# Kernel optimization log

Hardware: AMD Instinct MI355X
Metric: run time of the kernel (lower is better)

## Reference

```python
import jax, jax.numpy as jnp
import numpy as np

NUM_ITERATIONS = 100
EPS = 1e-6
LIPSCHITZ_COEFF = 0.9


def _l2_normalize(x, axis=None, eps=1e-12):
    return x * jax.lax.rsqrt((x * x).sum(axis=axis, keepdims=True) + eps)


def setup_inputs() -> dict:
    key = jax.random.key(0)
    k1, k2, k3, k4 = jax.random.split(key, 4)
    B, D_in, D_out = 32768, 1024, 1024
    x = jax.random.normal(k1, (B, D_in), dtype=jnp.float32)
    # TruncatedNormal(stddev=1/sqrt(fan_in)) approximated by scaled normal
    w = jax.random.normal(k2, (D_in, D_out), dtype=jnp.float32) / np.sqrt(D_in)
    b = jax.random.normal(k3, (D_out,), dtype=jnp.float32)
    u0 = jax.random.normal(k4, (1, D_out), dtype=jnp.float32)
    return {"x": x, "w": w, "b": b, "u0": u0}


def reference(x, w, b, u0):
    d_in = w.shape[0]

    # 100-step power iteration: tight sequential dependency chain of GEMV pairs.
    def body(i, carry):
        u, _ = carry
        v = _l2_normalize(jnp.matmul(u, w.T), eps=EPS)   # [1, d_in]
        u = _l2_normalize(jnp.matmul(v, w), eps=EPS)     # [1, d_out]
        return (u, v)

    v_init = jnp.zeros((1, d_in), dtype=w.dtype)
    u, v = jax.lax.fori_loop(0, NUM_ITERATIONS, body, (u0, v_init))
    u = jax.lax.stop_gradient(u)
    v = jax.lax.stop_gradient(v)

    sigma = jnp.matmul(jnp.matmul(v, w), u.T)[0, 0]      # spectral norm estimate
    factor = jnp.maximum(1.0, sigma / LIPSCHITZ_COEFF)
    w_norm = w / factor

    out = jnp.dot(x, w_norm) + b
    return out
```

## Files before the change

kernel.cpp:

```cpp
#include <hip/hip_runtime.h>
#include <hip/hip_bf16.h>
#include <cstdint>
#include <cstddef>

#define DDIM 1024
#define BROWS 32768

typedef __attribute__((ext_vector_type(8))) short short8;
typedef __attribute__((ext_vector_type(4))) float floatx4;

__device__ __forceinline__ float bf2f(unsigned short u) {
  return __uint_as_float(((unsigned int)u) << 16);
}
__device__ __forceinline__ unsigned short f2bf(float f) {
  unsigned int u = __float_as_uint(f);
  u += 0x7FFFu + ((u >> 16) & 1u);
  return (unsigned short)(u >> 16);
}

__device__ __forceinline__ void load_lds16(const void* g, void* l) {
  __builtin_amdgcn_global_load_lds(
      (const __attribute__((address_space(1))) unsigned int*)g,
      (__attribute__((address_space(3))) unsigned int*)l,
      16, 0, 0);
}

__global__ void __launch_bounds__(512, 2)
big_gemm(const float* __restrict__ Af, const unsigned short* __restrict__ Bt,
         float* __restrict__ Outf, const float* __restrict__ inv_ptr,
         const float* __restrict__ bias)
{
  __shared__ __align__(16) char smem[49152];

  const int tid  = threadIdx.x;
  const int lane = tid & 63;
  const int wid  = tid >> 6;
  const int wr = wid >> 2, wc = wid & 3;
  const int g = lane >> 4, r = lane & 15;

  const int bm0 = (int)(blockIdx.x & 255) * 128;
  const int bn0 = (int)(blockIdx.x >> 8) * 256;

  const floatx4 zero4 = {0.f, 0.f, 0.f, 0.f};
  floatx4 acc[4][4];
#pragma unroll
  for (int m = 0; m < 4; ++m)
#pragma unroll
    for (int n = 0; n < 4; ++n) acc[m][n] = zero4;

  const int ao   = tid * 16;
  const int arow = ao >> 6;
  const int acol = (ao & 63) >> 1;
  const float* aSrc = Af + (size_t)(bm0 + arow) * DDIM + acol;

  {
#pragma unroll
    for (int p = 0; p < 2; ++p) {
      const int o = p * 8192 + tid * 16;
      const int row = o >> 6;
      const int cole = (o & 63) >> 1;
      load_lds16(Bt + (size_t)(bn0 + row) * DDIM + cole, smem + 16384 + o);
    }
    float4 x0 = *(const float4*)aSrc;
    float4 x1 = *(const float4*)(aSrc + 4);
    short8 t;
    t[0] = (short)f2bf(x0.x); t[1] = (short)f2bf(x0.y);
    t[2] = (short)f2bf(x0.z); t[3] = (short)f2bf(x0.w);
    t[4] = (short)f2bf(x1.x); t[5] = (short)f2bf(x1.y);
    t[6] = (short)f2bf(x1.z); t[7] = (short)f2bf(x1.w);
    *(short8*)(smem + ao) = t;
  }
  __syncthreads();

  for (int t = 0; t < 32; ++t) {
    const int co = t & 1;
    char* curA = smem + co * 8192;
    char* curB = smem + 16384 + co * 16384;
    char* nxtA = smem + (co ^ 1) * 8192;
    char* nxtB = smem + 16384 + (co ^ 1) * 16384;

    float4 pa0, pa1;
    const bool pref = (t < 31);
    if (pref) {
      const int ko = (t + 1) * 32;
#pragma unroll
      for (int p = 0; p < 2; ++p) {
        const int o = p * 8192 + tid * 16;
        const int row = o >> 6;
        const int cole = (o & 63) >> 1;
        load_lds16(Bt + (size_t)(bn0 + row) * DDIM + ko + cole, nxtB + o);
      }
      pa0 = *(const float4*)(aSrc + ko);
      pa1 = *(const float4*)(aSrc + ko + 4);
    }

    short8 afr[4], bfr[4];
#pragma unroll
    for (int m = 0; m < 4; ++m)
      afr[m] = *(const short8*)(curA + (wr * 64 + m * 16 + r) * 64 + g * 16);
#pragma unroll
    for (int n = 0; n < 4; ++n)
      bfr[n] = *(const short8*)(curB + (wc * 64 + n * 16 + r) * 64 + g * 16);
#pragma unroll
    for (int m = 0; m < 4; ++m)
#pragma unroll
      for (int n = 0; n < 4; ++n)
        acc[m][n] = __builtin_amdgcn_mfma_f32_16x16x32_bf16(afr[m], bfr[n], acc[m][n], 0, 0, 0);

    if (pref) {
      short8 tt;
      tt[0] = (short)f2bf(pa0.x); tt[1] = (short)f2bf(pa0.y);
      tt[2] = (short)f2bf(pa0.z); tt[3] = (short)f2bf(pa0.w);
      tt[4] = (short)f2bf(pa1.x); tt[5] = (short)f2bf(pa1.y);
      tt[6] = (short)f2bf(pa1.z); tt[7] = (short)f2bf(pa1.w);
      *(short8*)(nxtA + ao) = tt;
    }
    __syncthreads();
  }

  const float inv = *inv_ptr;
#pragma unroll
  for (int n = 0; n < 4; ++n) {
    const int ocol = bn0 + wc * 64 + n * 16 + r;
    const float bv = bias[ocol];
#pragma unroll
    for (int m = 0; m < 4; ++m) {
      const int orow0 = bm0 + wr * 64 + m * 16 + g * 4;
#pragma unroll
      for (int q = 0; q < 4; ++q) {
        Outf[(size_t)(orow0 + q) * DDIM + ocol] = acc[m][n][q] * inv + bv;
      }
    }
  }
}

__global__ void __launch_bounds__(256, 2)
sq_gemm(const unsigned short* __restrict__ A, const unsigned short* __restrict__ Bt,
        unsigned short* __restrict__ Out, const float* __restrict__ in_max,
        float* __restrict__ out_max)
{
  __shared__ __align__(16) unsigned short As[2][4096];
  __shared__ __align__(16) unsigned short Bs[2][4096];
  __shared__ float redw[4];

  const int tid  = threadIdx.x;
  const int lane = tid & 63;
  const int wid  = tid >> 6;
  const int wr = wid >> 1, wc = wid & 1;
  const int g = lane >> 4, r = lane & 15;

  const int bm0 = (int)(blockIdx.x >> 4) * 64;
  const int bn0 = (int)(blockIdx.x & 15) * 64;

  const int so    = tid * 16;
  const int srow0 = so >> 7;
  const int sc16  = (so >> 4) & 7;
  const int scs   = sc16 ^ (srow0 & 7);
  const unsigned short* aSrc0 = A  + (size_t)(bm0 + srow0) * DDIM + scs * 8;
  const unsigned short* aSrc1 = A  + (size_t)(bm0 + 32 + srow0) * DDIM + scs * 8;
  const unsigned short* bSrc0 = Bt + (size_t)(bn0 + srow0) * DDIM + scs * 8;
  const unsigned short* bSrc1 = Bt + (size_t)(bn0 + 32 + srow0) * DDIM + scs * 8;

  const floatx4 zero4 = {0.f, 0.f, 0.f, 0.f};
  floatx4 acc[2][2];
#pragma unroll
  for (int fm = 0; fm < 2; ++fm)
#pragma unroll
    for (int fn = 0; fn < 2; ++fn) acc[fm][fn] = zero4;

  load_lds16(aSrc0, (char*)&As[0][0] + so);
  load_lds16(aSrc1, (char*)&As[0][0] + 4096 + so);
  load_lds16(bSrc0, (char*)&Bs[0][0] + so);
  load_lds16(bSrc1, (char*)&Bs[0][0] + 4096 + so);
  __syncthreads();

  int buf = 0;
  for (int t = 0; t < 16; ++t) {
    if (t + 1 < 16) {
      const int kk = (t + 1) * 64;
      load_lds16(aSrc0 + kk, (char*)&As[buf ^ 1][0] + so);
      load_lds16(aSrc1 + kk, (char*)&As[buf ^ 1][0] + 4096 + so);
      load_lds16(bSrc0 + kk, (char*)&Bs[buf ^ 1][0] + so);
      load_lds16(bSrc1 + kk, (char*)&Bs[buf ^ 1][0] + 4096 + so);
    }
#pragma unroll
    for (int ks = 0; ks < 2; ++ks) {
      const int chunk = ((ks << 2) + g) ^ (r & 7);
      short8 af[2], bf[2];
#pragma unroll
      for (int fm = 0; fm < 2; ++fm) {
        const int arow = wr * 32 + fm * 16 + r;
        af[fm] = *(const short8*)((const char*)&As[buf][0] + (arow << 7) + (chunk << 4));
      }
#pragma unroll
      for (int fn = 0; fn < 2; ++fn) {
        const int brow = wc * 32 + fn * 16 + r;
        bf[fn] = *(const short8*)((const char*)&Bs[buf][0] + (brow << 7) + (chunk << 4));
      }
#pragma unroll
      for (int fm = 0; fm < 2; ++fm)
#pragma unroll
        for (int fn = 0; fn < 2; ++fn)
          acc[fm][fn] = __builtin_amdgcn_mfma_f32_16x16x32_bf16(af[fm], bf[fn], acc[fm][fn], 0, 0, 0);
    }
    __syncthreads();
    buf ^= 1;
  }

  float c = 1.0f;
  if (in_max != nullptr) {
    int e;
    (void)frexpf(*in_max, &e);
    c = ldexpf(1.0f, -e);
  }
  const float c2 = c * c;
  float lmax = 0.0f;
#pragma unroll
  for (int fm = 0; fm < 2; ++fm) {
#pragma unroll
    for (int fn = 0; fn < 2; ++fn) {
      const int ocol = bn0 + wc * 32 + fn * 16 + r;
#pragma unroll
      for (int q = 0; q < 4; ++q) {
        const int orow = bm0 + wr * 32 + fm * 16 + g * 4 + q;
        float v = acc[fm][fn][q] * c2;
        Out[(size_t)orow * DDIM + ocol] = f2bf(v);
        lmax = fmaxf(lmax, fabsf(v));
      }
    }
  }
#pragma unroll
  for (int off = 32; off > 0; off >>= 1) lmax = fmaxf(lmax, __shfl_down(lmax, off));
  if (lane == 0) redw[wid] = lmax;
  __syncthreads();
  if (tid == 0) {
    float m = fmaxf(fmaxf(redw[0], redw[1]), fmaxf(redw[2], redw[3]));
    atomicMax((unsigned int*)out_max, __float_as_uint(m));
  }
}

__global__ void __launch_bounds__(256)
transpose_bf16(const float* __restrict__ W, unsigned short* __restrict__ WT)
{
  __shared__ float tile[64][65];
  const int bx = blockIdx.x & 15;
  const int by = blockIdx.x >> 4;
  const int tid = threadIdx.x;
  const int c = tid & 63;
  const int r0 = tid >> 6;
#pragma unroll
  for (int p = 0; p < 16; ++p) {
    int kr = p * 4 + r0;
    tile[kr][c] = W[(size_t)(bx * 64 + kr) * DDIM + by * 64 + c];
  }
  __syncthreads();
#pragma unroll
  for (int p = 0; p < 16; ++p) {
    int nr = p * 4 + r0;
    WT[(size_t)(by * 64 + nr) * DDIM + bx * 64 + c] = f2bf(tile[c][nr]);
  }
}

__global__ void __launch_bounds__(256)
gemv_pow(const unsigned short* __restrict__ P, const float* __restrict__ vin,
         float* __restrict__ vout)
{
  const int tid = threadIdx.x;
  const int lane = tid & 63;
  const int wid = tid >> 6;
  float vs[16];
  const float4* vv = (const float4*)(vin + lane * 16);
#pragma unroll
  for (int i = 0; i < 4; ++i) {
    float4 t = vv[i];
    vs[i * 4 + 0] = t.x; vs[i * 4 + 1] = t.y; vs[i * 4 + 2] = t.z; vs[i * 4 + 3] = t.w;
  }
#pragma unroll
  for (int rr = 0; rr < 4; ++rr) {
    const int row = (int)blockIdx.x * 16 + wid * 4 + rr;
    const unsigned short* pr = P + (size_t)row * DDIM + lane * 16;
    short8 p0 = *(const short8*)pr;
    short8 p1 = *(const short8*)(pr + 8);
    float s = 0.f;
#pragma unroll
    for (int e = 0; e < 8; ++e) s += bf2f((unsigned short)p0[e]) * vs[e];
#pragma unroll
    for (int e = 0; e < 8; ++e) s += bf2f((unsigned short)p1[e]) * vs[8 + e];
#pragma unroll
    for (int off = 32; off > 0; off >>= 1) s += __shfl_down(s, off);
    if (lane == 0) vout[row] = s * 0x1p-12f;
  }
}

__global__ void __launch_bounds__(256)
v_kernel(const float* __restrict__ W, const float* __restrict__ d,
         float* __restrict__ v_un, float* __restrict__ vpart)
{
  __shared__ float wsum[4];
  const int tid = threadIdx.x;
  const int lane = tid & 63;
  const int wid = tid >> 6;
  float vs[16];
  const float4* dv = (const float4*)(d + lane * 16);
#pragma unroll
  for (int i = 0; i < 4; ++i) {
    float4 t = dv[i];
    vs[i * 4 + 0] = t.x; vs[i * 4 + 1] = t.y; vs[i * 4 + 2] = t.z; vs[i * 4 + 3] = t.w;
  }
  float ssq = 0.f;
#pragma unroll
  for (int rr = 0; rr < 4; ++rr) {
    const int row = (int)blockIdx.x * 16 + wid * 4 + rr;
    const float4* wrow = (const float4*)(W + (size_t)row * DDIM + lane * 16);
    float s = 0.f;
#pragma unroll
    for (int i = 0; i < 4; ++i) {
      float4 t = wrow[i];
      s += t.x * vs[i * 4 + 0] + t.y * vs[i * 4 + 1] + t.z * vs[i * 4 + 2] + t.w * vs[i * 4 + 3];
    }
#pragma unroll
    for (int off = 32; off > 0; off >>= 1) s += __shfl_down(s, off);
    if (lane == 0) { v_un[row] = s; ssq += s * s; }
  }
  if (lane == 0) wsum[wid] = ssq;
  __syncthreads();
  if (tid == 0) vpart[blockIdx.x] = (wsum[0] + wsum[1]) + (wsum[2] + wsum[3]);
}

__global__ void __launch_bounds__(256)
t_fin_kernel(const float* __restrict__ W, const float* __restrict__ v_un,
             float* __restrict__ vpart, float* __restrict__ tpart,
             unsigned int* __restrict__ counter, float* __restrict__ inv_out)
{
  __shared__ float part[8][33];
  __shared__ unsigned int sticket;
  const int tid = threadIdx.x;
  const int col = (int)blockIdx.x * 32 + (tid & 31);
  const int ch = tid >> 5;
  float s = 0.f;
  const int i0 = ch * 128;
  for (int i = i0; i < i0 + 128; ++i)
    s += v_un[i] * W[(size_t)i * DDIM + col];
  part[ch][tid & 31] = s;
  __syncthreads();
  if (tid < 32) {
    float t = 0.f;
#pragma unroll
    for (int c2 = 0; c2 < 8; ++c2) t += part[c2][tid];
    part[0][tid] = t * t;
  }
  __syncthreads();
  if (tid == 0) {
    float ss = 0.f;
#pragma unroll
    for (int c = 0; c < 32; ++c) ss += part[0][c];
    tpart[blockIdx.x] = ss;
    __threadfence();
    sticket = atomicAdd(counter, 1u);
  }
  __syncthreads();
  if (sticket == 31) {
    __threadfence();
    float val = 0.f;
    if (tid < 64)
      val = __uint_as_float(atomicOr((unsigned int*)&vpart[tid], 0u));
    part[tid >> 5][tid & 31] = val;
    __syncthreads();
    if (tid == 0) {
      float sv = 0.f;
      for (int i = 0; i < 64; ++i) sv += part[i >> 5][i & 31];
      float stq = 0.f;
      for (int i = 0; i < 32; ++i)
        stq += __uint_as_float(atomicOr((unsigned int*)&tpart[i], 0u));
      float sigma = sqrtf(stq / sv);
      inv_out[0] = (sigma > 0.9f) ? (0.9f / sigma) : 1.0f;
    }
  }
}

extern "C" void kernel_launch(void* const* d_in, const int* in_sizes, int n_in,
                              void* d_out, int out_size, void* d_ws, size_t ws_size,
                              hipStream_t stream)
{
  const float* x  = (const float*)d_in[0];
  const float* w  = (const float*)d_in[1];
  const float* b  = (const float*)d_in[2];
  const float* u0 = (const float*)d_in[3];
  float* out = (float*)d_out;

  char* ws = (char*)d_ws;
  float* scal = (float*)ws;
  float* u_a  = (float*)(ws + 0x1000);
  float* u_b  = (float*)(ws + 0x2000);
  float* v_un = (float*)(ws + 0x3000);
  unsigned short* WT = (unsigned short*)(ws + 0x4000);
  unsigned short* P0 = (unsigned short*)(ws + 0x204000);
  unsigned short* P1 = (unsigned short*)(ws + 0x404000);

  hipMemsetAsync(d_ws, 0, 4096, stream);
  hipLaunchKernelGGL(transpose_bf16, dim3(256), dim3(256), 0, stream, w, WT);

  hipLaunchKernelGGL(sq_gemm, dim3(256), dim3(256), 0, stream,
                     WT, WT, P0, (const float*)nullptr, &scal[0]);
  hipLaunchKernelGGL(sq_gemm, dim3(256), dim3(256), 0, stream,
                     P0, P0, P1, &scal[0], &scal[1]);
  hipLaunchKernelGGL(sq_gemm, dim3(256), dim3(256), 0, stream,
                     P1, P1, P0, &scal[1], &scal[2]);
  hipLaunchKernelGGL(sq_gemm, dim3(256), dim3(256), 0, stream,
                     P0, P0, P1, &scal[2], &scal[3]);
  hipLaunchKernelGGL(sq_gemm, dim3(256), dim3(256), 0, stream,
                     P1, P1, P0, &scal[3], &scal[4]);
  hipLaunchKernelGGL(sq_gemm, dim3(256), dim3(256), 0, stream,
                     P0, P0, P1, &scal[4], &scal[5]);

  hipLaunchKernelGGL(gemv_pow, dim3(64), dim3(256), 0, stream, P1, u0, u_a);
  hipLaunchKernelGGL(gemv_pow, dim3(64), dim3(256), 0, stream, P1, u_a, u_b);
  hipLaunchKernelGGL(gemv_pow, dim3(64), dim3(256), 0, stream, P1, u_b, u_a);

  hipLaunchKernelGGL(v_kernel, dim3(64), dim3(256), 0, stream, w, u_a, v_un, &scal[16]);
  hipLaunchKernelGGL(t_fin_kernel, dim3(32), dim3(256), 0, stream,
                     w, v_un, &scal[16], &scal[80],
                     (unsigned int*)&scal[120], &scal[8]);

  hipLaunchKernelGGL(big_gemm, dim3(1024), dim3(512), 0, stream,
                     x, WT, out, &scal[8], b);
}
```

Measured before the change: 225.2 us.

## Prefetch fp32 A tiles two stages ahead with fine-grained vmcnt waits

The big GEMM now loads fp32 A data for tile t+2 into registers while tile t+1 is converted to bf16 and stored to LDS. The blanket __syncthreads is replaced with manual s_waitcnt vmcnt(2) plus s_barrier, so the in-flight A loads are not drained at each barrier. Bias and the scale factor are also loaded at kernel start rather than in the epilogue. In exchange it holds more registers live, and correctness depends on hand-counted vmcnt values.

```diff
diff --git a/kernel.cpp b/kernel.cpp
--- a/kernel.cpp
+++ b/kernel.cpp
@@ -41,6 +41,11 @@
   const int bm0 = (int)(blockIdx.x & 255) * 128;
   const int bn0 = (int)(blockIdx.x >> 8) * 256;
 
+  const float inv = *inv_ptr;
+  float bv[4];
+#pragma unroll
+  for (int n = 0; n < 4; ++n) bv[n] = bias[bn0 + wc * 64 + n * 16 + r];
+
   const floatx4 zero4 = {0.f, 0.f, 0.f, 0.f};
   floatx4 acc[4][4];
 #pragma unroll
@@ -63,14 +68,18 @@
     }
     float4 x0 = *(const float4*)aSrc;
     float4 x1 = *(const float4*)(aSrc + 4);
-    short8 t;
-    t[0] = (short)f2bf(x0.x); t[1] = (short)f2bf(x0.y);
-    t[2] = (short)f2bf(x0.z); t[3] = (short)f2bf(x0.w);
-    t[4] = (short)f2bf(x1.x); t[5] = (short)f2bf(x1.y);
-    t[6] = (short)f2bf(x1.z); t[7] = (short)f2bf(x1.w);
-    *(short8*)(smem + ao) = t;
-  }
-  __syncthreads();
+    short8 t0;
+    t0[0] = (short)f2bf(x0.x); t0[1] = (short)f2bf(x0.y);
+    t0[2] = (short)f2bf(x0.z); t0[3] = (short)f2bf(x0.w);
+    t0[4] = (short)f2bf(x1.x); t0[5] = (short)f2bf(x1.y);
+    t0[6] = (short)f2bf(x1.z); t0[7] = (short)f2bf(x1.w);
+    *(short8*)(smem + ao) = t0;
+  }
+  float4 aC0 = *(const float4*)(aSrc + 32);
+  float4 aC1 = *(const float4*)(aSrc + 36);
+  asm volatile("s_waitcnt vmcnt(2) lgkmcnt(0)" ::: "memory");
+  __builtin_amdgcn_sched_barrier(0);
+  __builtin_amdgcn_s_barrier();
 
   for (int t = 0; t < 32; ++t) {
     const int co = t & 1;
@@ -79,9 +88,7 @@
     char* nxtA = smem + (co ^ 1) * 8192;
     char* nxtB = smem + 16384 + (co ^ 1) * 16384;
 
-    float4 pa0, pa1;
-    const bool pref = (t < 31);
-    if (pref) {
+    if (t + 1 < 32) {
       const int ko = (t + 1) * 32;
 #pragma unroll
       for (int p = 0; p < 2; ++p) {
@@ -90,8 +97,12 @@
         const int cole = (o & 63) >> 1;
         load_lds16(Bt + (size_t)(bn0 + row) * DDIM + ko + cole, nxtB + o);
       }
-      pa0 = *(const float4*)(aSrc + ko);
-      pa1 = *(const float4*)(aSrc + ko + 4);
+    }
+    float4 aN0, aN1;
+    if (t + 2 < 32) {
+      const int ko2 = (t + 2) * 32;
+      aN0 = *(const float4*)(aSrc + ko2);
+      aN1 = *(const float4*)(aSrc + ko2 + 4);
     }
 
     short8 afr[4], bfr[4];
@@ -107,28 +118,36 @@
       for (int n = 0; n < 4; ++n)
         acc[m][n] = __builtin_amdgcn_mfma_f32_16x16x32_bf16(afr[m], bfr[n], acc[m][n], 0, 0, 0);
 
-    if (pref) {
+    if (t + 1 < 32) {
       short8 tt;
-      tt[0] = (short)f2bf(pa0.x); tt[1] = (short)f2bf(pa0.y);
-      tt[2] = (short)f2bf(pa0.z); tt[3] = (short)f2bf(pa0.w);
-      tt[4] = (short)f2bf(pa1.x); tt[5] = (short)f2bf(pa1.y);
-      tt[6] = (short)f2bf(pa1.z); tt[7] = (short)f2bf(pa1.w);
+      tt[0] = (short)f2bf(aC0.x); tt[1] = (short)f2bf(aC0.y);
+      tt[2] = (short)f2bf(aC0.z); tt[3] = (short)f2bf(aC0.w);
+      tt[4] = (short)f2bf(aC1.x); tt[5] = (short)f2bf(aC1.y);
+      tt[6] = (short)f2bf(aC1.z); tt[7] = (short)f2bf(aC1.w);
       *(short8*)(nxtA + ao) = tt;
     }
-    __syncthreads();
-  }
-
-  const float inv = *inv_ptr;
+
+    if (t < 31) {
+      if (t < 30) {
+        asm volatile("s_waitcnt vmcnt(2) lgkmcnt(0)" ::: "memory");
+      } else {
+        asm volatile("s_waitcnt vmcnt(0) lgkmcnt(0)" ::: "memory");
+      }
+      __builtin_amdgcn_sched_barrier(0);
+      __builtin_amdgcn_s_barrier();
+    }
+    aC0 = aN0; aC1 = aN1;
+  }
+
 #pragma unroll
   for (int n = 0; n < 4; ++n) {
     const int ocol = bn0 + wc * 64 + n * 16 + r;
-    const float bv = bias[ocol];
 #pragma unroll
     for (int m = 0; m < 4; ++m) {
       const int orow0 = bm0 + wr * 64 + m * 16 + g * 4;
 #pragma unroll
       for (int q = 0; q < 4; ++q) {
-        Outf[(size_t)(orow0 + q) * DDIM + ocol] = acc[m][n][q] * inv + bv;
+        Outf[(size_t)(orow0 + q) * DDIM + ocol] = acc[m][n][q] * inv + bv[n];
       }
     }
   }
```

After: 255.7 us. 1.14x slower.
